# Optimization experiments

Measured on AMD Instinct MI355X. Metric: run time of the kernel, lower is better.

The kernel has to match this reference:

```python
import jax, jax.numpy as jnp
import numpy as np

LAYER_NUMS = 3
# activations per layer: elu, elu, none (matches expert_activations=["elu","elu",null])
ACTS = [jax.nn.elu, jax.nn.elu, None]


def setup_inputs() -> dict:
    key = jax.random.key(0)
    k1, k2, k3, k4 = jax.random.split(key, 4)
    E, D, B_ = 8, 2048, 4096
    weight_blend = jax.random.uniform(k1, (E,), dtype=jnp.float32)
    x = jax.random.normal(k2, (B_, D), dtype=jnp.float32)
    W = jax.random.normal(k3, (LAYER_NUMS, E, D, D), dtype=jnp.float32) * 0.02
    B = jax.random.normal(k4, (LAYER_NUMS, D), dtype=jnp.float32) * 0.02
    return {"weight_blend": weight_blend, "x": x, "W": W, "B": B}


def reference(weight_blend, x, W, B):
    # Dropout is identity in eval/deterministic mode (expert_keep_prob=0.0).
    for i in range(LAYER_NUMS):
        # blended weight: sum_e c_e * W_e  -> (out, in)
        w = jnp.einsum("e,eoi->oi", weight_blend, W[i])
        x = x @ w.T + B[i]
        if ACTS[i] is not None:
            x = ACTS[i](x)
    return x
```

## Files before the change

kernel.cpp:

```cpp
#include <hip/hip_runtime.h>
#include <hip/hip_bf16.h>

#define MDIM 4096
#define NDIM 2048
#define KDIM 2048
#define KTILES 32
#define PER_LAYER 4194304

typedef __attribute__((ext_vector_type(8))) short bf16x8;
typedef __attribute__((ext_vector_type(4))) float f32x4;

__device__ __forceinline__ unsigned short f2bf(float f) {
    unsigned u = __builtin_bit_cast(unsigned, f);
    u += 0x7FFFu + ((u >> 16) & 1u);
    return (unsigned short)(u >> 16);
}

__global__ __launch_bounds__(256) void blend0_kernel(
    const float* __restrict__ W, const float* __restrict__ cb,
    const float* __restrict__ x,
    unsigned short* __restrict__ wb, unsigned short* __restrict__ xb)
{
    float c[8];
#pragma unroll
    for (int e = 0; e < 8; ++e) c[e] = cb[e];
    const unsigned wtotal4 = PER_LAYER >> 2;
    const unsigned xtotal4 = 2097152u;
    const unsigned total = wtotal4 + xtotal4;
    unsigned stride = gridDim.x * blockDim.x;
    for (unsigned i = blockIdx.x * blockDim.x + threadIdx.x; i < total; i += stride) {
        if (i < wtotal4) {
            unsigned off = i << 2;
            const float* base = W + off;
            float4 s = make_float4(0.f, 0.f, 0.f, 0.f);
#pragma unroll
            for (int e = 0; e < 8; ++e) {
                float4 v = *(const float4*)(base + (size_t)e * PER_LAYER);
                s.x += c[e] * v.x; s.y += c[e] * v.y;
                s.z += c[e] * v.z; s.w += c[e] * v.w;
            }
            ushort4 o;
            o.x = f2bf(s.x); o.y = f2bf(s.y); o.z = f2bf(s.z); o.w = f2bf(s.w);
            *(ushort4*)(wb + off) = o;
        } else {
            unsigned j = (i - wtotal4) << 2;
            float4 v = *(const float4*)(x + j);
            ushort4 o;
            o.x = f2bf(v.x); o.y = f2bf(v.y); o.z = f2bf(v.z); o.w = f2bf(v.w);
            *(ushort4*)(xb + j) = o;
        }
    }
}

#define BARR() do { asm volatile("" ::: "memory"); __builtin_amdgcn_s_barrier(); asm volatile("" ::: "memory"); } while (0)
#define SP(N) __builtin_amdgcn_s_setprio(N)
#define VMC_IMPL(N) asm volatile("s_waitcnt vmcnt(" #N ")" ::: "memory")
#define VMC(N) VMC_IMPL(N)

template<int ACT, typename OutT, int BLEND>
__global__ __launch_bounds__(512, 2) void gemm_fused(
    const unsigned short* __restrict__ A,
    const unsigned short* __restrict__ Bw,
    const float* __restrict__ bias,
    OutT* __restrict__ C,
    const float* __restrict__ Wnext,
    const float* __restrict__ cb,
    unsigned short* __restrict__ wbNext)
{
    __shared__ __align__(16) unsigned short lds[73728];
    char* ldsc = (char*)lds;

    const int tid = threadIdx.x;
    const int wid = tid >> 6;
    const int lane = tid & 63;
    const int wr = wid >> 1;
    const int wc = wid & 1;

    float cw[8];
    if (BLEND) {
#pragma unroll
        for (int e = 0; e < 8; ++e) cw[e] = cb[e];
        VMC(0);
    }

    const int wg = (blockIdx.x & 7) * 32 + (blockIdx.x >> 3);
    const size_t blockM = (size_t)(wg & 15) * 256;
    const size_t blockN = (size_t)(wg >> 4) * 128;

    const int sw = (lane & 7) << 4;
    const int ck = (lane >> 4) << 4;
    const int rAb = wr * 64 + (lane & 15);
    const int rBb = wc * 64 + (lane & 15);

    const int srow = tid >> 3;
    const int scol = ((tid & 7) ^ (srow & 7)) << 3;
    const unsigned short* aStage = A + (blockM + srow) * KDIM + scol;
    const unsigned short* bStage = Bw + (blockN + srow) * KDIM + scol;

#define STAGE_AS(BUF, S, KT) do { \
    const unsigned short* g_ = aStage + (size_t)(S) * 64 * KDIM + (size_t)(KT) * 64; \
    __builtin_amdgcn_global_load_lds((const __attribute__((address_space(1))) void*)g_, \
        (__attribute__((address_space(3))) void*)(ldsc + (BUF) * 49152 + (S) * 8192 + tid * 16), \
        16, 0, 0); \
} while (0)

#define STAGE_BS(BUF, S, KT) do { \
    const unsigned short* g_ = bStage + (size_t)(S) * 64 * KDIM + (size_t)(KT) * 64; \
    __builtin_amdgcn_global_load_lds((const __attribute__((address_space(1))) void*)g_, \
        (__attribute__((address_space(3))) void*)(ldsc + (BUF) * 49152 + 32768 + (S) * 8192 + tid * 16), \
        16, 0, 0); \
} while (0)

#define RD_A(BUF, M, KK) \
    (*(const bf16x8*)(ldsc + (BUF) * 49152 + ((rAb + (M) * 16)) * 128 + (((KK) * 64 + ck) ^ sw)))
#define RD_B(BUF, N, KK) \
    (*(const bf16x8*)(ldsc + (BUF) * 49152 + 32768 + (rBb + (N) * 16) * 128 + (((KK) * 64 + ck) ^ sw)))

    f32x4 acc[4][4];
#pragma unroll
    for (int m = 0; m < 4; ++m)
#pragma unroll
        for (int n = 0; n < 4; ++n) acc[m][n] = (f32x4){0.f, 0.f, 0.f, 0.f};

#define GEMM_ITER(T, WAITER) do { \
    int stb_ = cur + 2; if (stb_ >= 3) stb_ -= 3; \
    bf16x8 af[4][2], bfr[4][2]; \
    _Pragma("unroll") for (int m_ = 0; m_ < 4; ++m_) { \
        af[m_][0] = RD_A(cur, m_, 0); af[m_][1] = RD_A(cur, m_, 1); } \
    _Pragma("unroll") for (int n_ = 0; n_ < 4; ++n_) { \
        bfr[n_][0] = RD_B(cur, n_, 0); bfr[n_][1] = RD_B(cur, n_, 1); } \
    if ((T) + 2 < KTILES) { \
        STAGE_AS(stb_, 0, (T) + 2); STAGE_AS(stb_, 1, (T) + 2); \
        STAGE_AS(stb_, 2, (T) + 2); STAGE_AS(stb_, 3, (T) + 2); \
        STAGE_BS(stb_, 0, (T) + 2); STAGE_BS(stb_, 1, (T) + 2); \
    } \
    SP(1); \
    _Pragma("unroll") for (int kk_ = 0; kk_ < 2; ++kk_) \
    _Pragma("unroll") for (int m_ = 0; m_ < 4; ++m_) \
    _Pragma("unroll") for (int n_ = 0; n_ < 4; ++n_) \
        acc[m_][n_] = __builtin_amdgcn_mfma_f32_16x16x32_bf16( \
            af[m_][kk_], bfr[n_][kk_], acc[m_][n_], 0, 0, 0); \
    SP(0); \
    WAITER; \
    BARR(); \
    cur = cur + 1; if (cur >= 3) cur = 0; \
} while (0)

#define BLEND_STEP(G) do { \
    const unsigned idx_ = (unsigned)(G) * 131072u + (unsigned)blockIdx.x * 512u + (unsigned)tid; \
    const unsigned off_ = idx_ << 2; \
    const float* bs_ = Wnext + off_; \
    float4 s_ = make_float4(0.f, 0.f, 0.f, 0.f); \
    _Pragma("unroll") for (int e_ = 0; e_ < 8; ++e_) { \
        float4 v_ = *(const float4*)(bs_ + (size_t)e_ * PER_LAYER); \
        s_.x += cw[e_] * v_.x; s_.y += cw[e_] * v_.y; \
        s_.z += cw[e_] * v_.z; s_.w += cw[e_] * v_.w; } \
    ushort4 o_; \
    o_.x = f2bf(s_.x); o_.y = f2bf(s_.y); o_.z = f2bf(s_.z); o_.w = f2bf(s_.w); \
    *(ushort4*)(wbNext + off_) = o_; \
} while (0)

    STAGE_AS(0, 0, 0); STAGE_AS(0, 1, 0); STAGE_AS(0, 2, 0); STAGE_AS(0, 3, 0);
    STAGE_BS(0, 0, 0); STAGE_BS(0, 1, 0);
    STAGE_AS(1, 0, 1); STAGE_AS(1, 1, 1); STAGE_AS(1, 2, 1); STAGE_AS(1, 3, 1);
    STAGE_BS(1, 0, 1); STAGE_BS(1, 1, 1);
    VMC(6);
    BARR();

    int cur = 0;
    if (BLEND) {
#pragma unroll 1
        for (int g = 0; g < 8; ++g) {
            const int t0 = 3 * g;
            GEMM_ITER(t0, VMC(6));
            BLEND_STEP(g);
            GEMM_ITER(t0 + 1, VMC(15));
            GEMM_ITER(t0 + 2, VMC(6));
        }
#pragma unroll 1
        for (int t = 24; t < 30; ++t) GEMM_ITER(t, VMC(6));
    } else {
#pragma unroll 1
        for (int t = 0; t < 30; ++t) GEMM_ITER(t, VMC(6));
    }
    GEMM_ITER(30, VMC(0));
    GEMM_ITER(31, VMC(0));

    const int crow = (lane >> 4) * 4;
    const int ccol = lane & 15;
#pragma unroll
    for (int m = 0; m < 4; ++m)
#pragma unroll
        for (int n = 0; n < 4; ++n) {
            const size_t col = blockN + wc * 64 + n * 16 + ccol;
            const float bv = bias[col];
#pragma unroll
            for (int r = 0; r < 4; ++r) {
                const size_t row = blockM + wr * 64 + m * 16 + crow + r;
                float v = acc[m][n][r] + bv;
                if (ACT) v = v > 0.f ? v : expm1f(v);
                if constexpr (sizeof(OutT) == 2) {
                    C[row * NDIM + col] = (OutT)f2bf(v);
                } else {
                    C[row * NDIM + col] = (OutT)v;
                }
            }
        }
#undef STAGE_AS
#undef STAGE_BS
#undef RD_A
#undef RD_B
#undef GEMM_ITER
#undef BLEND_STEP
}

extern "C" void kernel_launch(void* const* d_in, const int* in_sizes, int n_in,
                              void* d_out, int out_size, void* d_ws, size_t ws_size,
                              hipStream_t stream) {
    const float* blendw = (const float*)d_in[0];
    const float* x      = (const float*)d_in[1];
    const float* W      = (const float*)d_in[2];
    const float* Bb     = (const float*)d_in[3];
    float* out = (float*)d_out;

    unsigned short* wb0 = (unsigned short*)d_ws;
    unsigned short* wb1 = wb0 + PER_LAYER;
    unsigned short* wb2 = wb1 + PER_LAYER;
    unsigned short* xb  = wb2 + PER_LAYER;
    unsigned short* y0  = xb + 8388608;
    unsigned short* y1  = xb;

    blend0_kernel<<<2048, 256, 0, stream>>>(W, blendw, x, wb0, xb);

    gemm_fused<1, unsigned short, 1><<<256, 512, 0, stream>>>(
        xb, wb0, Bb,        y0,  W + (size_t)8 * PER_LAYER,  blendw, wb1);
    gemm_fused<1, unsigned short, 1><<<256, 512, 0, stream>>>(
        y0, wb1, Bb + 2048, y1,  W + (size_t)16 * PER_LAYER, blendw, wb2);
    gemm_fused<0, float, 0><<<256, 512, 0, stream>>>(
        y1, wb2, Bb + 4096, out, nullptr, nullptr, nullptr);
}
```

Before: 204.8 us.

## Store blended weights in MFMA fragment order and load B directly to registers

The blend kernels now write the bf16 weight matrix in a pre-swizzled MFMA B-fragment layout, so the GEMM can load B fragments straight from global memory into registers, double-buffered across iterations, instead of staging them through LDS. This drops the B portion of shared memory (LDS per block falls from 144KB to 96KB), along with the associated LDS reads, and spreads the next-layer blend work evenly as one step every four iterations. The cost is that each wave fetches B from global or L2 with no LDS sharing. Wave pairs that share columns now load the same B data twice, and the global load latency has to be covered by a single iteration of prefetch.

```diff
diff --git a/kernel.cpp b/kernel.cpp
--- a/kernel.cpp
+++ b/kernel.cpp
@@ -14,6 +14,11 @@
     unsigned u = __builtin_bit_cast(unsigned, f);
     u += 0x7FFFu + ((u >> 16) & 1u);
     return (unsigned short)(u >> 16);
+}
+
+__device__ __forceinline__ unsigned bfrag_off(unsigned n, unsigned k) {
+    return ((n >> 4) * 64u + (k >> 5)) * 512u
+         + (((n & 15u) + (((k >> 3) & 3u) << 4)) << 3) + (k & 7u);
 }
 
 __global__ __launch_bounds__(256) void blend0_kernel(
@@ -41,7 +46,7 @@
             }
             ushort4 o;
             o.x = f2bf(s.x); o.y = f2bf(s.y); o.z = f2bf(s.z); o.w = f2bf(s.w);
-            *(ushort4*)(wb + off) = o;
+            *(ushort4*)(wb + bfrag_off(off >> 11, off & 2047u)) = o;
         } else {
             unsigned j = (i - wtotal4) << 2;
             float4 v = *(const float4*)(x + j);
@@ -58,7 +63,7 @@
 #define VMC(N) VMC_IMPL(N)
 
 template<int ACT, typename OutT, int BLEND>
-__global__ __launch_bounds__(512, 2) void gemm_fused(
+__global__ __launch_bounds__(512, 2) void gemm_bfrag(
     const unsigned short* __restrict__ A,
     const unsigned short* __restrict__ Bw,
     const float* __restrict__ bias,
@@ -67,7 +72,7 @@
     const float* __restrict__ cb,
     unsigned short* __restrict__ wbNext)
 {
-    __shared__ __align__(16) unsigned short lds[73728];
+    __shared__ __align__(16) unsigned short lds[49152];
     char* ldsc = (char*)lds;
 
     const int tid = threadIdx.x;
@@ -90,31 +95,31 @@
     const int sw = (lane & 7) << 4;
     const int ck = (lane >> 4) << 4;
     const int rAb = wr * 64 + (lane & 15);
-    const int rBb = wc * 64 + (lane & 15);
 
     const int srow = tid >> 3;
     const int scol = ((tid & 7) ^ (srow & 7)) << 3;
     const unsigned short* aStage = A + (blockM + srow) * KDIM + scol;
-    const unsigned short* bStage = Bw + (blockN + srow) * KDIM + scol;
-
-#define STAGE_AS(BUF, S, KT) do { \
+
+    const unsigned short* bBase =
+        Bw + ((size_t)((blockN >> 4) + wc * 4) * 64) * 512 + lane * 8;
+
+#define STAGE_A(BUF, S, KT) do { \
     const unsigned short* g_ = aStage + (size_t)(S) * 64 * KDIM + (size_t)(KT) * 64; \
     __builtin_amdgcn_global_load_lds((const __attribute__((address_space(1))) void*)g_, \
-        (__attribute__((address_space(3))) void*)(ldsc + (BUF) * 49152 + (S) * 8192 + tid * 16), \
+        (__attribute__((address_space(3))) void*)(ldsc + (BUF) * 32768 + (S) * 8192 + tid * 16), \
         16, 0, 0); \
 } while (0)
 
-#define STAGE_BS(BUF, S, KT) do { \
-    const unsigned short* g_ = bStage + (size_t)(S) * 64 * KDIM + (size_t)(KT) * 64; \
-    __builtin_amdgcn_global_load_lds((const __attribute__((address_space(1))) void*)g_, \
-        (__attribute__((address_space(3))) void*)(ldsc + (BUF) * 49152 + 32768 + (S) * 8192 + tid * 16), \
-        16, 0, 0); \
+#define STAGE_A4(BUF, KT) do { \
+    STAGE_A(BUF, 0, KT); STAGE_A(BUF, 1, KT); STAGE_A(BUF, 2, KT); STAGE_A(BUF, 3, KT); \
 } while (0)
 
 #define RD_A(BUF, M, KK) \
-    (*(const bf16x8*)(ldsc + (BUF) * 49152 + ((rAb + (M) * 16)) * 128 + (((KK) * 64 + ck) ^ sw)))
-#define RD_B(BUF, N, KK) \
-    (*(const bf16x8*)(ldsc + (BUF) * 49152 + 32768 + (rBb + (N) * 16) * 128 + (((KK) * 64 + ck) ^ sw)))
+    (*(const bf16x8*)(ldsc + (BUF) * 32768 + (rAb + (M) * 16) * 128 + (((KK) * 64 + ck) ^ sw)))
+
+#define LOAD_B(DST, T) do { _Pragma("unroll") for (int n_ = 0; n_ < 4; ++n_) { \
+    DST[n_][0] = *(const bf16x8*)(bBase + (size_t)n_ * 32768 + (size_t)(T) * 1024); \
+    DST[n_][1] = *(const bf16x8*)(bBase + (size_t)n_ * 32768 + (size_t)(T) * 1024 + 512); } } while (0)
 
     f32x4 acc[4][4];
 #pragma unroll
@@ -122,29 +127,7 @@
 #pragma unroll
         for (int n = 0; n < 4; ++n) acc[m][n] = (f32x4){0.f, 0.f, 0.f, 0.f};
 
-#define GEMM_ITER(T, WAITER) do { \
-    int stb_ = cur + 2; if (stb_ >= 3) stb_ -= 3; \
-    bf16x8 af[4][2], bfr[4][2]; \
-    _Pragma("unroll") for (int m_ = 0; m_ < 4; ++m_) { \
-        af[m_][0] = RD_A(cur, m_, 0); af[m_][1] = RD_A(cur, m_, 1); } \
-    _Pragma("unroll") for (int n_ = 0; n_ < 4; ++n_) { \
-        bfr[n_][0] = RD_B(cur, n_, 0); bfr[n_][1] = RD_B(cur, n_, 1); } \
-    if ((T) + 2 < KTILES) { \
-        STAGE_AS(stb_, 0, (T) + 2); STAGE_AS(stb_, 1, (T) + 2); \
-        STAGE_AS(stb_, 2, (T) + 2); STAGE_AS(stb_, 3, (T) + 2); \
-        STAGE_BS(stb_, 0, (T) + 2); STAGE_BS(stb_, 1, (T) + 2); \
-    } \
-    SP(1); \
-    _Pragma("unroll") for (int kk_ = 0; kk_ < 2; ++kk_) \
-    _Pragma("unroll") for (int m_ = 0; m_ < 4; ++m_) \
-    _Pragma("unroll") for (int n_ = 0; n_ < 4; ++n_) \
-        acc[m_][n_] = __builtin_amdgcn_mfma_f32_16x16x32_bf16( \
-            af[m_][kk_], bfr[n_][kk_], acc[m_][n_], 0, 0, 0); \
-    SP(0); \
-    WAITER; \
-    BARR(); \
-    cur = cur + 1; if (cur >= 3) cur = 0; \
-} while (0)
+    bf16x8 bE[4][2], bO[4][2];
 
 #define BLEND_STEP(G) do { \
     const unsigned idx_ = (unsigned)(G) * 131072u + (unsigned)blockIdx.x * 512u + (unsigned)tid; \
@@ -157,34 +140,43 @@
         s_.z += cw[e_] * v_.z; s_.w += cw[e_] * v_.w; } \
     ushort4 o_; \
     o_.x = f2bf(s_.x); o_.y = f2bf(s_.y); o_.z = f2bf(s_.z); o_.w = f2bf(s_.w); \
-    *(ushort4*)(wbNext + off_) = o_; \
-} while (0)
-
-    STAGE_AS(0, 0, 0); STAGE_AS(0, 1, 0); STAGE_AS(0, 2, 0); STAGE_AS(0, 3, 0);
-    STAGE_BS(0, 0, 0); STAGE_BS(0, 1, 0);
-    STAGE_AS(1, 0, 1); STAGE_AS(1, 1, 1); STAGE_AS(1, 2, 1); STAGE_AS(1, 3, 1);
-    STAGE_BS(1, 0, 1); STAGE_BS(1, 1, 1);
-    VMC(6);
+    *(ushort4*)(wbNext + bfrag_off(off_ >> 11, off_ & 2047u)) = o_; \
+} while (0)
+
+#define GEMM_ITER(T, BCUR, BNXT, WAITER) do { \
+    int stb_ = cur + 2; if (stb_ >= 3) stb_ -= 3; \
+    bf16x8 af[4][2]; \
+    _Pragma("unroll") for (int m_ = 0; m_ < 4; ++m_) { \
+        af[m_][0] = RD_A(cur, m_, 0); af[m_][1] = RD_A(cur, m_, 1); } \
+    if (BLEND && ((T) & 3) == 0) BLEND_STEP((T) >> 2); \
+    if ((T) + 1 < KTILES) LOAD_B(BNXT, (T) + 1); \
+    if ((T) + 2 < KTILES) STAGE_A4(stb_, (T) + 2); \
+    SP(1); \
+    _Pragma("unroll") for (int kk_ = 0; kk_ < 2; ++kk_) \
+    _Pragma("unroll") for (int m_ = 0; m_ < 4; ++m_) \
+    _Pragma("unroll") for (int n_ = 0; n_ < 4; ++n_) \
+        acc[m_][n_] = __builtin_amdgcn_mfma_f32_16x16x32_bf16( \
+            af[m_][kk_], BCUR[n_][kk_], acc[m_][n_], 0, 0, 0); \
+    SP(0); \
+    WAITER; \
+    BARR(); \
+    cur = cur + 1; if (cur >= 3) cur = 0; \
+} while (0)
+
+    STAGE_A4(0, 0);
+    LOAD_B(bE, 0);
+    STAGE_A4(1, 1);
+    VMC(4);
     BARR();
 
     int cur = 0;
-    if (BLEND) {
 #pragma unroll 1
-        for (int g = 0; g < 8; ++g) {
-            const int t0 = 3 * g;
-            GEMM_ITER(t0, VMC(6));
-            BLEND_STEP(g);
-            GEMM_ITER(t0 + 1, VMC(15));
-            GEMM_ITER(t0 + 2, VMC(6));
-        }
-#pragma unroll 1
-        for (int t = 24; t < 30; ++t) GEMM_ITER(t, VMC(6));
-    } else {
-#pragma unroll 1
-        for (int t = 0; t < 30; ++t) GEMM_ITER(t, VMC(6));
+    for (int t = 0; t < 30; t += 2) {
+        GEMM_ITER(t,     bE, bO, VMC(4));
+        GEMM_ITER(t + 1, bO, bE, VMC(4));
     }
-    GEMM_ITER(30, VMC(0));
-    GEMM_ITER(31, VMC(0));
+    GEMM_ITER(30, bE, bO, VMC(0));
+    GEMM_ITER(31, bO, bE, VMC(0));
 
     const int crow = (lane >> 4) * 4;
     const int ccol = lane & 15;
@@ -206,10 +198,10 @@
                 }
             }
         }
-#undef STAGE_AS
-#undef STAGE_BS
+#undef STAGE_A
+#undef STAGE_A4
 #undef RD_A
-#undef RD_B
+#undef LOAD_B
 #undef GEMM_ITER
 #undef BLEND_STEP
 }
@@ -232,10 +224,11 @@
 
     blend0_kernel<<<2048, 256, 0, stream>>>(W, blendw, x, wb0, xb);
 
-    gemm_fused<1, unsigned short, 1><<<256, 512, 0, stream>>>(
+    const int grid = (MDIM / 256) * (NDIM / 128);
+    gemm_bfrag<1, unsigned short, 1><<<grid, 512, 0, stream>>>(
         xb, wb0, Bb,        y0,  W + (size_t)8 * PER_LAYER,  blendw, wb1);
-    gemm_fused<1, unsigned short, 1><<<256, 512, 0, stream>>>(
+    gemm_bfrag<1, unsigned short, 1><<<grid, 512, 0, stream>>>(
         y0, wb1, Bb + 2048, y1,  W + (size_t)16 * PER_LAYER, blendw, wb2);
-    gemm_fused<0, float, 0><<<256, 512, 0, stream>>>(
+    gemm_bfrag<0, float, 0><<<grid, 512, 0, stream>>>(
         y1, wb2, Bb + 4096, out, nullptr, nullptr, nullptr);
 }
```

After: 248.3 us. 21.2% more time.
